# Kernel optimization log

Hardware: AMD Instinct MI355X
Metric: run time of the kernel (lower is better)

Reference implementation:

```python
import jax, jax.numpy as jnp
import numpy as np

N_NODES = 50000
N_EDGES = 800000
D_IN = 64
D_OUT = 64


def setup_inputs() -> dict:
    key = jax.random.key(0)
    k1, k2, k3, k4 = jax.random.split(key, 4)
    x = jax.random.normal(k1, (N_NODES, D_IN), dtype=jnp.float32)
    edge_index = jax.random.randint(k2, (2, N_EDGES), 0, N_NODES, dtype=jnp.int64)
    W = jax.random.normal(k3, (D_IN, D_OUT), dtype=jnp.float32) * (1.0 / np.sqrt(D_IN))
    b = jax.random.normal(k4, (D_OUT,), dtype=jnp.float32) * 0.01
    return {"x": x, "edge_index": edge_index, "W": W, "b": b}


def reference(x, edge_index, W, b):
    N = x.shape[0]
    # Add self-loops (PyG GCNConv default add_self_loops=True)
    loop = jnp.arange(N, dtype=edge_index.dtype)
    src = jnp.concatenate([edge_index[0], loop])  # source j
    dst = jnp.concatenate([edge_index[1], loop])  # target i
    # Linear transform first (standard GCNConv: theta then propagate)
    xw = x @ W  # [N, D_OUT]
    # Symmetric degree normalization: deg over targets of (A + I)
    ones = jnp.ones(src.shape[0], dtype=x.dtype)
    deg = jax.ops.segment_sum(ones, dst, num_segments=N)
    dis = jnp.where(deg > 0, jax.lax.rsqrt(jnp.maximum(deg, 1.0)), 0.0)
    norm = dis[src] * dis[dst]  # [E+N]
    # Gather, weight, scatter-add
    msgs = norm[:, None] * xw[src]  # [E+N, D_OUT]
    out = jax.ops.segment_sum(msgs, dst, num_segments=N) + b
    return jax.nn.relu(out)
```

## Files before the change

kernel.cpp:

```cpp
#include <hip/hip_runtime.h>

#define N_NODES 50000
#define N_EDGES 800000
#define D 64
#define FINE_SHIFT 6
#define NBUCK 782
#define CAP 1280
#define SEGCAP 64
#define EPB 8192
#define NPART 98
#define NMM 196
#define NSTART (NBUCK + 1)

typedef _Float16 f16;
typedef __attribute__((ext_vector_type(4))) _Float16 f16x4;
typedef __attribute__((ext_vector_type(8))) _Float16 f16x8;
typedef __attribute__((ext_vector_type(4))) float f32x4;

#define SMEM_PART (2 * NBUCK * 4 + EPB * 4)
#define SMEM_MM   (64 * 72 * 2 + 256 * 72 * 2)
#define SMEM_SZ   (SMEM_MM > SMEM_PART ? SMEM_MM : SMEM_PART)

__global__ __launch_bounds__(1024) void partition_matmul(
    const int* __restrict__ src, const int* __restrict__ dst,
    unsigned int* __restrict__ binned2, int* __restrict__ starts2,
    const float* __restrict__ W, const float* __restrict__ x,
    f16* __restrict__ xwh)
{
    __shared__ __align__(16) unsigned char smem[SMEM_SZ];
    int tid = threadIdx.x;

    if (blockIdx.x >= NPART) {
        f16 (*WtH)[72]  = (f16 (*)[72])smem;
        f16 (*park)[72] = (f16 (*)[72])(smem + 64 * 72 * 2);

        for (int j = tid; j < 4096; j += 1024)
            WtH[j & 63][j >> 6] = (f16)W[j];
        __syncthreads();

        int nb = (blockIdx.x - NPART) * 256;
        int wave = tid >> 6, lane = tid & 63;
        int m = lane & 15, q = lane >> 4;

        int ar = nb + wave * 16 + m;
        if (ar >= N_NODES) ar = N_NODES - 1;
        const float4* x4 = (const float4*)x;
        size_t rb = (size_t)ar * 16;
        float4 p0 = x4[rb + q * 2];
        float4 p1 = x4[rb + q * 2 + 1];
        float4 p2 = x4[rb + 8 + q * 2];
        float4 p3 = x4[rb + 8 + q * 2 + 1];
        f16x8 a0 = { (f16)p0.x, (f16)p0.y, (f16)p0.z, (f16)p0.w,
                     (f16)p1.x, (f16)p1.y, (f16)p1.z, (f16)p1.w };
        f16x8 a1 = { (f16)p2.x, (f16)p2.y, (f16)p2.z, (f16)p2.w,
                     (f16)p3.x, (f16)p3.y, (f16)p3.z, (f16)p3.w };

        f32x4 acc[4];
        #pragma unroll
        for (int t = 0; t < 4; ++t) {
            int n0 = t * 16;
            f16x8 b0 = *(const f16x8*)&WtH[n0 + m][q * 8];
            f16x8 b1 = *(const f16x8*)&WtH[n0 + m][32 + q * 8];
            f32x4 z = { 0.f, 0.f, 0.f, 0.f };
            z = __builtin_amdgcn_mfma_f32_16x16x32_f16(a0, b0, z, 0, 0, 0);
            acc[t] = __builtin_amdgcn_mfma_f32_16x16x32_f16(a1, b1, z, 0, 0, 0);
        }

        #pragma unroll
        for (int t = 0; t < 4; ++t) {
            int n0 = t * 16;
            #pragma unroll
            for (int r = 0; r < 4; ++r)
                park[wave * 16 + q * 4 + r][n0 + m] = (f16)acc[t][r];
        }
        __syncthreads();

        for (int j = tid; j < 2048; j += 1024) {
            int row = j >> 3, seg = (j & 7) * 8;
            int n = nb + row;
            if (n < N_NODES)
                *(f16x8*)&xwh[(size_t)n * D + seg] = *(const f16x8*)&park[row][seg];
        }
        return;
    }

    int* hist            = (int*)smem;
    int* start_s         = hist + NBUCK;
    unsigned int* staged = (unsigned int*)(start_s + NBUCK);

    int eb  = blockIdx.x * EPB;
    int total = N_EDGES - eb; if (total > EPB) total = EPB;

    for (int i = tid; i < NBUCK; i += 1024) hist[i] = 0;
    __syncthreads();

    unsigned int rec[8];
    int rank[8];
    int jb = tid * 8;
    if (jb < total) {
        int4 s0 = *(const int4*)&src[eb + jb];
        int4 s1 = *(const int4*)&src[eb + jb + 4];
        int4 d0 = *(const int4*)&dst[eb + jb];
        int4 d1 = *(const int4*)&dst[eb + jb + 4];
        rec[0] = ((unsigned)d0.x << 16) | (unsigned)s0.x;
        rec[1] = ((unsigned)d0.y << 16) | (unsigned)s0.y;
        rec[2] = ((unsigned)d0.z << 16) | (unsigned)s0.z;
        rec[3] = ((unsigned)d0.w << 16) | (unsigned)s0.w;
        rec[4] = ((unsigned)d1.x << 16) | (unsigned)s1.x;
        rec[5] = ((unsigned)d1.y << 16) | (unsigned)s1.y;
        rec[6] = ((unsigned)d1.z << 16) | (unsigned)s1.z;
        rec[7] = ((unsigned)d1.w << 16) | (unsigned)s1.w;
        #pragma unroll
        for (int u = 0; u < 8; ++u)
            rank[u] = atomicAdd(&hist[rec[u] >> (16 + FINE_SHIFT)], 1);
    } else {
        #pragma unroll
        for (int u = 0; u < 8; ++u) rec[u] = 0xFFFFFFFFu;
    }
    __syncthreads();

    if (tid < 64) {
        int b0 = tid * 13;
        int v[13]; int run = 0;
        #pragma unroll
        for (int j = 0; j < 13; ++j) {
            int idx = b0 + j;
            int c = (idx < NBUCK) ? hist[idx] : 0;
            v[j] = run; run += c;
        }
        int s = run;
        #pragma unroll
        for (int off = 1; off < 64; off <<= 1) {
            int t = __shfl_up(s, off);
            if (tid >= off) s += t;
        }
        int excl = s - run;
        #pragma unroll
        for (int j = 0; j < 13; ++j) {
            int idx = b0 + j;
            if (idx < NBUCK) start_s[idx] = excl + v[j];
        }
    }
    __syncthreads();

    #pragma unroll
    for (int u = 0; u < 8; ++u) {
        unsigned int v = rec[u];
        if (v != 0xFFFFFFFFu)
            staged[start_s[v >> 22] + rank[u]] = v;
    }
    __syncthreads();

    for (int i = tid; i < total; i += 1024)
        binned2[(size_t)blockIdx.x * EPB + i] = staged[i];
    for (int i = tid; i < NBUCK; i += 1024)
        starts2[(size_t)blockIdx.x * NSTART + i] = start_s[i];
    if (tid == 0)
        starts2[(size_t)blockIdx.x * NSTART + NBUCK] = total;
}

__global__ __launch_bounds__(256) void degree_dis(
    const unsigned int* __restrict__ binned2, const int* __restrict__ starts2,
    float* __restrict__ dis)
{
    __shared__ int h[64];
    __shared__ int segoff_s[NPART], segcnt_s[NPART];

    int bu = blockIdx.x, tid = threadIdx.x;
    if (tid < 64) h[tid] = 0;
    if (tid < NPART) {
        size_t base = (size_t)tid * NSTART + bu;
        int s0 = starts2[base], s1 = starts2[base + 1];
        int c = s1 - s0; if (c < 0) c = 0; if (c > SEGCAP) c = SEGCAP;
        segoff_s[tid] = s0; segcnt_s[tid] = c;
    }
    __syncthreads();

    int wave = tid >> 6, lane = tid & 63;
    for (int blk = wave; blk < NPART; blk += 4) {
        int c = segcnt_s[blk];
        if (lane < c) {
            unsigned int r = binned2[(size_t)blk * EPB + segoff_s[blk] + lane];
            atomicAdd(&h[(r >> 16) & 63], 1);
        }
    }
    __syncthreads();

    int n = bu * 64 + tid;
    if (tid < 64 && n < N_NODES)
        dis[n] = rsqrtf((float)h[tid] + 1.0f);
}

__global__ __launch_bounds__(512) void gather_out(
    const unsigned int* __restrict__ binned2, const int* __restrict__ starts2,
    const f16* __restrict__ xwh, const float* __restrict__ dis,
    const float* __restrict__ b, float* __restrict__ out)
{
    __shared__ unsigned int srec[CAP];
    __shared__ unsigned short ssrc[CAP];
    __shared__ int h[64], off_s[64], cur[64];
    __shared__ int segoff_s[NPART], segcnt_s[NPART], segbase_s[NPART];
    __shared__ int stot_s;

    int cb = blockIdx.x, tid = threadIdx.x;
    int wave = tid >> 6, lane = tid & 63;
    int nb = cb * 64;

    if (tid < 64) h[tid] = 0;
    if (tid < NPART) {
        size_t base = (size_t)tid * NSTART + cb;
        int s0 = starts2[base], s1 = starts2[base + 1];
        int c = s1 - s0; if (c < 0) c = 0; if (c > SEGCAP) c = SEGCAP;
        segoff_s[tid] = s0; segcnt_s[tid] = c;
    }
    __syncthreads();

    if (tid < 64) {
        int v0 = segcnt_s[tid], s = v0;
        #pragma unroll
        for (int off = 1; off < 64; off <<= 1) {
            int t = __shfl_up(s, off);
            if (tid >= off) s += t;
        }
        segbase_s[tid] = s - v0;
        int T0 = __shfl(s, 63);
        int v1 = (tid < NPART - 64) ? segcnt_s[64 + tid] : 0;
        int s1 = v1;
        #pragma unroll
        for (int off = 1; off < 64; off <<= 1) {
            int t = __shfl_up(s1, off);
            if (tid >= off) s1 += t;
        }
        if (tid < NPART - 64) segbase_s[64 + tid] = T0 + s1 - v1;
        int T1 = __shfl(s1, 63);
        if (tid == 0) {
            int tot = T0 + T1; if (tot > CAP) tot = CAP;
            stot_s = tot;
        }
    }
    __syncthreads();

    for (int blk = wave; blk < NPART; blk += 8) {
        int c = segcnt_s[blk];
        if (lane < c) {
            int p = segbase_s[blk] + lane;
            if (p < CAP)
                srec[p] = binned2[(size_t)blk * EPB + segoff_s[blk] + lane];
        }
    }
    __syncthreads();
    int cnt = stot_s;

    unsigned int rec[3];
    #pragma unroll
    for (int u = 0; u < 3; ++u) {
        int j = u * 512 + tid;
        if (j < cnt) {
            rec[u] = srec[j];
            atomicAdd(&h[(rec[u] >> 16) & 63], 1);
        } else rec[u] = 0xFFFFFFFFu;
    }
    __syncthreads();

    if (tid < 64) {
        int v = h[tid], s = v;
        #pragma unroll
        for (int off = 1; off < 64; off <<= 1) {
            int t = __shfl_up(s, off);
            if (tid >= off) s += t;
        }
        off_s[tid] = s - v;
        cur[tid]   = s - v;
    }
    __syncthreads();

    #pragma unroll
    for (int u = 0; u < 3; ++u) {
        unsigned int v = rec[u];
        if (v != 0xFFFFFFFFu) {
            int p = atomicAdd(&cur[(v >> 16) & 63], 1);
            ssrc[p] = (unsigned short)(v & 0xFFFFu);
        }
    }
    __syncthreads();

    const f16x4* xw4 = (const f16x4*)xwh;
    const float4* b4p = (const float4*)b;
    float4* out4 = (float4*)out;
    int g = lane >> 4, c16 = lane & 15;

    for (int i = 0; i < 8; ++i) {
        int nl = wave * 8 + i;
        int n  = nb + nl;
        if (n >= N_NODES) break;
        int off = off_s[nl], c = h[nl];
        float dn = rsqrtf((float)c + 1.0f);

        float a0 = 0.f, a1 = 0.f, a2 = 0.f, a3 = 0.f;
        if (g == 0) {
            f16x4 sv = xw4[(size_t)n * 16 + c16];
            a0 = dn * (float)sv.x; a1 = dn * (float)sv.y;
            a2 = dn * (float)sv.z; a3 = dn * (float)sv.w;
        }
        int k = off + g, e = off + c;
        for (; k + 12 < e; k += 16) {
            int s0 = ssrc[k], s1 = ssrc[k + 4], s2 = ssrc[k + 8], s3 = ssrc[k + 12];
            float d0 = dis[s0], d1 = dis[s1], d2 = dis[s2], d3 = dis[s3];
            f16x4 v0 = xw4[(size_t)s0 * 16 + c16];
            f16x4 v1 = xw4[(size_t)s1 * 16 + c16];
            f16x4 v2 = xw4[(size_t)s2 * 16 + c16];
            f16x4 v3 = xw4[(size_t)s3 * 16 + c16];
            a0 = fmaf(d0, (float)v0.x, a0); a1 = fmaf(d0, (float)v0.y, a1);
            a2 = fmaf(d0, (float)v0.z, a2); a3 = fmaf(d0, (float)v0.w, a3);
            a0 = fmaf(d1, (float)v1.x, a0); a1 = fmaf(d1, (float)v1.y, a1);
            a2 = fmaf(d1, (float)v1.z, a2); a3 = fmaf(d1, (float)v1.w, a3);
            a0 = fmaf(d2, (float)v2.x, a0); a1 = fmaf(d2, (float)v2.y, a1);
            a2 = fmaf(d2, (float)v2.z, a2); a3 = fmaf(d2, (float)v2.w, a3);
            a0 = fmaf(d3, (float)v3.x, a0); a1 = fmaf(d3, (float)v3.y, a1);
            a2 = fmaf(d3, (float)v3.z, a2); a3 = fmaf(d3, (float)v3.w, a3);
        }
        for (; k + 4 < e; k += 8) {
            int s0 = ssrc[k], s1 = ssrc[k + 4];
            float d0 = dis[s0], d1 = dis[s1];
            f16x4 v0 = xw4[(size_t)s0 * 16 + c16];
            f16x4 v1 = xw4[(size_t)s1 * 16 + c16];
            a0 = fmaf(d0, (float)v0.x, a0); a1 = fmaf(d0, (float)v0.y, a1);
            a2 = fmaf(d0, (float)v0.z, a2); a3 = fmaf(d0, (float)v0.w, a3);
            a0 = fmaf(d1, (float)v1.x, a0); a1 = fmaf(d1, (float)v1.y, a1);
            a2 = fmaf(d1, (float)v1.z, a2); a3 = fmaf(d1, (float)v1.w, a3);
        }
        if (k < e) {
            int s = ssrc[k];
            float d = dis[s];
            f16x4 v = xw4[(size_t)s * 16 + c16];
            a0 = fmaf(d, (float)v.x, a0); a1 = fmaf(d, (float)v.y, a1);
            a2 = fmaf(d, (float)v.z, a2); a3 = fmaf(d, (float)v.w, a3);
        }
        a0 += __shfl_xor(a0, 32); a1 += __shfl_xor(a1, 32);
        a2 += __shfl_xor(a2, 32); a3 += __shfl_xor(a3, 32);
        a0 += __shfl_xor(a0, 16); a1 += __shfl_xor(a1, 16);
        a2 += __shfl_xor(a2, 16); a3 += __shfl_xor(a3, 16);
        if (g == 0) {
            float4 bl = b4p[c16];
            float4 r;
            r.x = fmaxf(bl.x + dn * a0, 0.f);
            r.y = fmaxf(bl.y + dn * a1, 0.f);
            r.z = fmaxf(bl.z + dn * a2, 0.f);
            r.w = fmaxf(bl.w + dn * a3, 0.f);
            out4[(size_t)n * 16 + c16] = r;
        }
    }
}

extern "C" void kernel_launch(void* const* d_in, const int* in_sizes, int n_in,
                              void* d_out, int out_size, void* d_ws, size_t ws_size,
                              hipStream_t stream) {
    const float* x  = (const float*)d_in[0];
    const int*   ei = (const int*)d_in[1];
    const float* W  = (const float*)d_in[2];
    const float* b  = (const float*)d_in[3];

    const int* src = ei;
    const int* dst = ei + N_EDGES;
    float* out = (float*)d_out;

    f16*          xwh     = (f16*)d_ws;
    unsigned int* binned2 = (unsigned int*)(xwh + (size_t)N_NODES * D);
    int*          starts2 = (int*)(binned2 + (size_t)NPART * EPB);
    float*        dis     = (float*)(starts2 + (size_t)NPART * NSTART);

    partition_matmul<<<NPART + NMM, 1024, 0, stream>>>(
        src, dst, binned2, starts2, W, x, xwh);
    degree_dis<<<NBUCK, 256, 0, stream>>>(binned2, starts2, dis);
    gather_out<<<NBUCK, 512, 0, stream>>>(binned2, starts2, xwh, dis, b, out);
}
```

Baseline: 115.5 us.

## Compact per-bucket edge records in degree pass and read contiguously in gather

The degree kernel now also gathers each bucket's scattered per-partition segments into a contiguous per-bucket array, using a binary search over segment bases, and records the count. The gather kernel then reads that contiguous array instead of redoing the segment-offset prefix scans and the strided 98-segment gather. This removes duplicated segment bookkeeping and the scattered loads from gather_out. In exchange it adds an extra global write and read of the edge records, plus binary-search overhead in the compaction step.

```diff
diff --git a/kernel.cpp b/kernel.cpp
--- a/kernel.cpp
+++ b/kernel.cpp
@@ -159,56 +159,20 @@
         starts2[(size_t)blockIdx.x * NSTART + NBUCK] = total;
 }
 
-__global__ __launch_bounds__(256) void degree_dis(
+__global__ __launch_bounds__(512) void compact_degree(
     const unsigned int* __restrict__ binned2, const int* __restrict__ starts2,
+    unsigned int* __restrict__ binned, int* __restrict__ cntc,
     float* __restrict__ dis)
 {
+    __shared__ int segcnt_s[NPART], segbase_s[NPART], segsrc_s[NPART];
+    __shared__ int segoff_s[NPART];
     __shared__ int h[64];
-    __shared__ int segoff_s[NPART], segcnt_s[NPART];
-
-    int bu = blockIdx.x, tid = threadIdx.x;
+    __shared__ int stot_s;
+
+    int cb = blockIdx.x, tid = threadIdx.x;
     if (tid < 64) h[tid] = 0;
     if (tid < NPART) {
-        size_t base = (size_t)tid * NSTART + bu;
-        int s0 = starts2[base], s1 = starts2[base + 1];
-        int c = s1 - s0; if (c < 0) c = 0; if (c > SEGCAP) c = SEGCAP;
-        segoff_s[tid] = s0; segcnt_s[tid] = c;
-    }
-    __syncthreads();
-
-    int wave = tid >> 6, lane = tid & 63;
-    for (int blk = wave; blk < NPART; blk += 4) {
-        int c = segcnt_s[blk];
-        if (lane < c) {
-            unsigned int r = binned2[(size_t)blk * EPB + segoff_s[blk] + lane];
-            atomicAdd(&h[(r >> 16) & 63], 1);
-        }
-    }
-    __syncthreads();
-
-    int n = bu * 64 + tid;
-    if (tid < 64 && n < N_NODES)
-        dis[n] = rsqrtf((float)h[tid] + 1.0f);
-}
-
-__global__ __launch_bounds__(512) void gather_out(
-    const unsigned int* __restrict__ binned2, const int* __restrict__ starts2,
-    const f16* __restrict__ xwh, const float* __restrict__ dis,
-    const float* __restrict__ b, float* __restrict__ out)
-{
-    __shared__ unsigned int srec[CAP];
-    __shared__ unsigned short ssrc[CAP];
-    __shared__ int h[64], off_s[64], cur[64];
-    __shared__ int segoff_s[NPART], segcnt_s[NPART], segbase_s[NPART];
-    __shared__ int stot_s;
-
-    int cb = blockIdx.x, tid = threadIdx.x;
-    int wave = tid >> 6, lane = tid & 63;
-    int nb = cb * 64;
-
-    if (tid < 64) h[tid] = 0;
-    if (tid < NPART) {
-        size_t base = (size_t)tid * NSTART + cb;
+        int base = tid * NSTART + cb;
         int s0 = starts2[base], s1 = starts2[base + 1];
         int c = s1 - s0; if (c < 0) c = 0; if (c > SEGCAP) c = SEGCAP;
         segoff_s[tid] = s0; segcnt_s[tid] = c;
@@ -239,24 +203,54 @@
         }
     }
     __syncthreads();
-
-    for (int blk = wave; blk < NPART; blk += 8) {
-        int c = segcnt_s[blk];
-        if (lane < c) {
-            int p = segbase_s[blk] + lane;
-            if (p < CAP)
-                srec[p] = binned2[(size_t)blk * EPB + segoff_s[blk] + lane];
-        }
-    }
-    __syncthreads();
-    int cnt = stot_s;
+    if (tid < NPART)
+        segsrc_s[tid] = tid * EPB + segoff_s[tid] - segbase_s[tid];
+    __syncthreads();
+
+    int stot = stot_s;
+    for (int i = tid; i < stot; i += 512) {
+        int lo = 0, hi = NPART - 1;
+        #pragma unroll
+        for (int it = 0; it < 7; ++it) {
+            int mid = (lo + hi + 1) >> 1;
+            if (segbase_s[mid] <= i) lo = mid; else hi = mid - 1;
+        }
+        unsigned int r = binned2[segsrc_s[lo] + i];
+        binned[(size_t)cb * CAP + i] = r;
+        atomicAdd(&h[(r >> 16) & 63], 1);
+    }
+    __syncthreads();
+
+    if (tid == 0) cntc[cb] = stot;
+    int n = cb * 64 + tid;
+    if (tid < 64 && n < N_NODES)
+        dis[n] = rsqrtf((float)h[tid] + 1.0f);
+}
+
+__global__ __launch_bounds__(512) void gather_out(
+    const int* __restrict__ cntc, const unsigned int* __restrict__ binned,
+    const f16* __restrict__ xwh, const float* __restrict__ dis,
+    const float* __restrict__ b, float* __restrict__ out)
+{
+    __shared__ unsigned short ssrc[CAP];
+    __shared__ int h[64], off_s[64], cur[64];
+
+    int cb = blockIdx.x, tid = threadIdx.x;
+    int wave = tid >> 6, lane = tid & 63;
+    int nb = cb * 64;
+    int cnt = cntc[cb];
+    if (cnt < 0) cnt = 0; if (cnt > CAP) cnt = CAP;
+    const unsigned int* br = binned + (size_t)cb * CAP;
+
+    if (tid < 64) h[tid] = 0;
+    __syncthreads();
 
     unsigned int rec[3];
     #pragma unroll
     for (int u = 0; u < 3; ++u) {
         int j = u * 512 + tid;
         if (j < cnt) {
-            rec[u] = srec[j];
+            rec[u] = br[j];
             atomicAdd(&h[(rec[u] >> 16) & 63], 1);
         } else rec[u] = 0xFFFFFFFFu;
     }
@@ -367,10 +361,12 @@
     f16*          xwh     = (f16*)d_ws;
     unsigned int* binned2 = (unsigned int*)(xwh + (size_t)N_NODES * D);
     int*          starts2 = (int*)(binned2 + (size_t)NPART * EPB);
-    float*        dis     = (float*)(starts2 + (size_t)NPART * NSTART);
+    unsigned int* binned  = (unsigned int*)(starts2 + (size_t)NPART * NSTART);
+    int*          cntc    = (int*)(binned + (size_t)NBUCK * CAP);
+    float*        dis     = (float*)(cntc + NBUCK);
 
     partition_matmul<<<NPART + NMM, 1024, 0, stream>>>(
         src, dst, binned2, starts2, W, x, xwh);
-    degree_dis<<<NBUCK, 256, 0, stream>>>(binned2, starts2, dis);
-    gather_out<<<NBUCK, 512, 0, stream>>>(binned2, starts2, xwh, dis, b, out);
+    compact_degree<<<NBUCK, 512, 0, stream>>>(binned2, starts2, binned, cntc, dis);
+    gather_out<<<NBUCK, 512, 0, stream>>>(cntc, binned, xwh, dis, b, out);
 }
```

Result: faster. 106.6 us (-7.7%).
